# Kernel tuning notes

Measured on AMD Instinct MI355X. Metric: run time of the kernel, lower is better.

## Reference

```python
import jax, jax.numpy as jnp
import numpy as np

N = 10000        # nodes
F_IN = 128       # node features (data.num_node_features)
OUT = 16         # out_channels
H = 32           # attention heads
C1 = 4 * OUT     # hidden per-head dim (4*out_channels)
E = 80000        # directed edges
EPS = 1e-5       # BatchNorm eps
NEG = 0.2        # GATConv LeakyReLU negative_slope


def _gat(x, src, dst, W, a_s, a_d, b, n, C):
    # PyG GATConv, shared lin, concat=False (mean over heads)
    h = (x @ W).reshape(n, H, C)                    # [n,H,C]
    e_src = jnp.sum(h * a_s, -1)                    # [n,H] (alpha from x_j)
    e_dst = jnp.sum(h * a_d, -1)                    # [n,H] (alpha from x_i)
    e = jax.nn.leaky_relu(e_src[src] + e_dst[dst], NEG)     # [E',H]
    m = jax.ops.segment_max(e, dst, num_segments=n)         # segment softmax
    p = jnp.exp(e - m[dst])
    z = jax.ops.segment_sum(p, dst, num_segments=n)
    alpha = p / z[dst]
    out = jax.ops.segment_sum(alpha[:, :, None] * h[src], dst, num_segments=n)
    return out.mean(1) + b                          # mean over heads + bias


def _bn(x, g, b, m, v):  # eval-mode BatchNorm1d (running stats)
    return (x - m) * g / jnp.sqrt(v + EPS) + b


def setup_inputs():
    k = jax.random.split(jax.random.key(0), 40)
    rn = lambda i, s, sc=0.1: jax.random.normal(k[i], s, jnp.float32) * sc
    d = {"x": jax.random.normal(k[0], (N, F_IN), jnp.float32),
         "edge_index": jax.random.randint(k[1], (2, E), 0, N, jnp.int32)}
    # 4 GATConv layers
    d.update(W1=rn(2, (F_IN, H * C1)), as1=rn(3, (H, C1)), ad1=rn(4, (H, C1)), b1=rn(5, (C1,)))
    d.update(W2=rn(6, (C1, H * OUT)), as2=rn(7, (H, OUT)), ad2=rn(8, (H, OUT)), b2=rn(9, (OUT,)))
    d.update(W3=rn(10, (F_IN, H * C1)), as3=rn(11, (H, C1)), ad3=rn(12, (H, C1)), b3=rn(13, (C1,)))
    d.update(W4=rn(14, (C1, H * OUT)), as4=rn(15, (H, OUT)), ad4=rn(16, (H, OUT)), b4=rn(17, (OUT,)))
    # ResidualNetwork(1 block): 1x1 Conv1d over L=1 == matmul
    d.update(rwa=rn(18, (F_IN, OUT)), rba=rn(19, (OUT,)),
             bn1g=jnp.ones(OUT), bn1b=jnp.zeros(OUT), bn1m=rn(20, (OUT,)), bn1v=jnp.abs(rn(21, (OUT,))) + 1.0,
             rwb=rn(22, (OUT, OUT)), rbb=rn(23, (OUT,)),
             bn2g=jnp.ones(OUT), bn2b=jnp.zeros(OUT), bn2m=rn(24, (OUT,)), bn2v=jnp.abs(rn(25, (OUT,))) + 1.0,
             wsc=rn(26, (F_IN, OUT)), bsc=rn(27, (OUT,)),
             bnsg=jnp.ones(OUT), bnsb=jnp.zeros(OUT), bnsm=rn(28, (OUT,)), bnsv=jnp.abs(rn(29, (OUT,))) + 1.0,
             wfc=rn(30, (OUT, OUT)), bfc=rn(31, (OUT,)))
    return d


def reference(x, edge_index, W1, as1, ad1, b1, W2, as2, ad2, b2,
              W3, as3, ad3, b3, W4, as4, ad4, b4,
              rwa, rba, bn1g, bn1b, bn1m, bn1v, rwb, rbb, bn2g, bn2b, bn2m, bn2v,
              wsc, bsc, bnsg, bnsb, bnsm, bnsv, wfc, bfc):
    n = x.shape[0]
    loops = jnp.arange(n, dtype=edge_index.dtype)  # add_self_loops=True
    s2t_src = jnp.concatenate([edge_index[0], loops])  # flow source_to_target
    s2t_dst = jnp.concatenate([edge_index[1], loops])
    t2s_src = jnp.concatenate([edge_index[1], loops])  # flow target_to_source
    t2s_dst = jnp.concatenate([edge_index[0], loops])
    # dropout in original is unassigned (no-op); eval mode assumed
    x_s = jax.nn.elu(_gat(x, s2t_src, s2t_dst, W1, as1, ad1, b1, n, C1))
    x_in = jax.nn.elu(_gat(x_s, s2t_src, s2t_dst, W2, as2, ad2, b2, n, OUT))
    x_t = jax.nn.elu(_gat(x, t2s_src, t2s_dst, W3, as3, ad3, b3, n, C1))
    x_out = jax.nn.elu(_gat(x_t, t2s_src, t2s_dst, W4, as4, ad4, b4, n, OUT))
    # ResidualNetwork: block + identity avg-pool (L=1) + fc
    h = jax.nn.relu(_bn(x @ rwa + rba, bn1g, bn1b, bn1m, bn1v))
    h = _bn(h @ rwb + rbb, bn2g, bn2b, bn2m, bn2v)
    sc = _bn(x @ wsc + bsc, bnsg, bnsb, bnsm, bnsv)
    x_self = jax.nn.relu(h + sc) @ wfc + bfc
    return (x_in, x_out, x_self)
```

## Files before the change

### kernel.cpp

```cpp
#include <hip/hip_runtime.h>
#include <stdint.h>

__device__ __forceinline__ float bf2f(unsigned short u) {
  union { unsigned int i; float f; } v; v.i = ((unsigned int)u) << 16; return v.f;
}
__device__ __forceinline__ unsigned short f2bf(float f) {
  union { float f; unsigned int i; } v; v.f = f;
  unsigned int i = v.i;
  unsigned int r = (i + 0x7fffu + ((i >> 16) & 1u)) >> 16;
  return (unsigned short)r;
}

typedef __bf16 bf16x8 __attribute__((ext_vector_type(8)));
typedef float f32x4 __attribute__((ext_vector_type(4)));
typedef float f32x2 __attribute__((ext_vector_type(2)));
union ABfrag { int4 i4; bf16x8 v; };

#if __has_builtin(__builtin_amdgcn_cvt_pk_fp8_f32) && __has_builtin(__builtin_amdgcn_cvt_pk_f32_fp8)
#define HW_FP8 1
#else
#define HW_FP8 0
#endif

__device__ __forceinline__ unsigned char f2fp8_sw(float f) {
  union { float f; unsigned int u; } v; v.f = f;
  unsigned int s = (v.u >> 24) & 0x80;
  float a = fabsf(f);
  if (a >= 448.f) return (unsigned char)(s | 0x7E);
  v.f = a;
  int ex = (int)(v.u >> 23);
  unsigned int man = v.u & 0x7FFFFFu;
  if (ex >= 121) {
    unsigned int val = ((unsigned int)(ex - 120) << 3) | (man >> 20);
    unsigned int rem = man & 0xFFFFFu;
    if (rem > 0x80000u || (rem == 0x80000u && (val & 1))) val++;
    if (val > 0x7E) val = 0x7E;
    return (unsigned char)(s | val);
  }
  int q = (int)(a * 512.f + 0.5f);
  if (q > 8) q = 8;
  return (unsigned char)(s | (unsigned int)q);
}
__device__ __forceinline__ float fp8dec_sw(unsigned char c) {
  unsigned int e = (c >> 3) & 15u, m = c & 7u;
  float v;
  if (e) { union { unsigned int u; float f; } x; x.u = ((e + 120) << 23) | (m << 20); v = x.f; }
  else v = (float)m * 0.001953125f;
  return (c & 0x80) ? -v : v;
}
__device__ __forceinline__ unsigned int pack4_fp8(float a0, float a1, float a2, float a3) {
#if HW_FP8
  int dw = __builtin_amdgcn_cvt_pk_fp8_f32(a0, a1, 0, false);
  dw = __builtin_amdgcn_cvt_pk_fp8_f32(a2, a3, dw, true);
  return (unsigned int)dw;
#else
  return (unsigned)f2fp8_sw(a0) | ((unsigned)f2fp8_sw(a1) << 8) |
         ((unsigned)f2fp8_sw(a2) << 16) | ((unsigned)f2fp8_sw(a3) << 24);
#endif
}
__device__ __forceinline__ unsigned int bytesel4(uint4 v, int rr) {
#if __has_builtin(__builtin_amdgcn_perm)
  unsigned s = (unsigned)rr | ((unsigned)(rr + 4) << 8);
  unsigned p01 = __builtin_amdgcn_perm(v.y, v.x, s);
  unsigned p23 = __builtin_amdgcn_perm(v.w, v.z, s);
  return __builtin_amdgcn_perm(p23, p01, 0x05040100u);
#else
  int sh = rr * 8;
  return ((v.x >> sh) & 0xFFu) | (((v.y >> sh) & 0xFFu) << 8) |
         (((v.z >> sh) & 0xFFu) << 16) | (((v.w >> sh) & 0xFFu) << 24);
#endif
}
__device__ __forceinline__ void dec16p(int4 g, f32x2 o[8]) {
#if HW_FP8
  o[0] = __builtin_amdgcn_cvt_pk_f32_fp8(g.x, false);
  o[1] = __builtin_amdgcn_cvt_pk_f32_fp8(g.x, true);
  o[2] = __builtin_amdgcn_cvt_pk_f32_fp8(g.y, false);
  o[3] = __builtin_amdgcn_cvt_pk_f32_fp8(g.y, true);
  o[4] = __builtin_amdgcn_cvt_pk_f32_fp8(g.z, false);
  o[5] = __builtin_amdgcn_cvt_pk_f32_fp8(g.z, true);
  o[6] = __builtin_amdgcn_cvt_pk_f32_fp8(g.w, false);
  o[7] = __builtin_amdgcn_cvt_pk_f32_fp8(g.w, true);
#else
  unsigned int w[4] = {(unsigned)g.x, (unsigned)g.y, (unsigned)g.z, (unsigned)g.w};
#pragma unroll
  for (int d = 0; d < 4; ++d) {
    unsigned int x = w[d];
    o[d * 2 + 0] = (f32x2){fp8dec_sw((unsigned char)(x & 0xFF)),
                           fp8dec_sw((unsigned char)((x >> 8) & 0xFF))};
    o[d * 2 + 1] = (f32x2){fp8dec_sw((unsigned char)((x >> 16) & 0xFF)),
                           fp8dec_sw((unsigned char)((x >> 24) & 0xFF))};
  }
#endif
}

__device__ __forceinline__ float lrelu_clamp(float e) {
  e = (e > 0.f) ? e : 0.2f * e;
  return fminf(e, 80.f);
}

__global__ __launch_bounds__(256) void k_detect(const unsigned int* __restrict__ x, int* flag,
                                                int* __restrict__ degAB, int ndeg2) {
  if (blockIdx.x == 0) {
    __shared__ int cnt;
    if (threadIdx.x == 0) cnt = 0;
    __syncthreads();
    int c = 0;
    for (int i = threadIdx.x; i < 1024; i += 256) {
      unsigned int lo = x[i] & 0xFFFFu;
      int ex = (int)((lo >> 7) & 0xFF);
      if (ex >= 100 && ex <= 140) c++;
    }
    atomicAdd(&cnt, c);
    __syncthreads();
    if (threadIdx.x == 0) flag[0] = (cnt > 600) ? 1 : 0;
    return;
  }
  for (int idx = (blockIdx.x - 1) * 256 + threadIdx.x; idx < ndeg2; idx += 8 * 256) degAB[idx] = 0;
}

struct PrepDesc {
  const void* csrc[32]; float* cdst[32]; int cn[32];
  const void* x; float* xc; unsigned short* xp;
  const void* W1; const void* W2; const void* W3; const void* W4;
  unsigned short* P1; unsigned short* P2; unsigned short* P3; unsigned short* P4;
  int* degAB;
  const int* ei;
  const void* av[4];
  float* wa[4];
  int nxb, xtotal, ctotal, E, nn;
};
__global__ __launch_bounds__(256) void k_prep(PrepDesc d, const int* __restrict__ flag) {
  int isbf = *flag;
  int b = blockIdx.x;
  if (b < d.nxb) {
    int t8 = b * 256 + threadIdx.x;
    int i8 = t8 * 8;
    if (i8 < d.xtotal) {
      float v[8];
      if (isbf) {
        int4 raw = *(const int4*)((const unsigned short*)d.x + i8);
        const unsigned short* u = (const unsigned short*)&raw;
#pragma unroll
        for (int j = 0; j < 8; ++j) v[j] = bf2f(u[j]);
      } else {
        float4 f0 = *(const float4*)((const float*)d.x + i8);
        float4 f1 = *(const float4*)((const float*)d.x + i8 + 4);
        v[0] = f0.x; v[1] = f0.y; v[2] = f0.z; v[3] = f0.w;
        v[4] = f1.x; v[5] = f1.y; v[6] = f1.z; v[7] = f1.w;
      }
      *(float4*)(d.xc + i8)     = (float4){v[0], v[1], v[2], v[3]};
      *(float4*)(d.xc + i8 + 4) = (float4){v[4], v[5], v[6], v[7]};
      int row = i8 >> 7, c0 = i8 & 127;
      int tm = row >> 4, mr = row & 15;
      int s = c0 >> 5, quad = (c0 >> 3) & 3;
      unsigned short o[8];
#pragma unroll
      for (int j = 0; j < 8; ++j) o[j] = f2bf(v[j]);
      size_t idx = (((size_t)tm * 4 + s) * 64 + quad * 16 + mr) * 8;
      *(int4*)(d.xp + idx) = *(const int4*)o;
    }
    return;
  }
  b -= d.nxb;
  if (b < 288) {
    int u = b * 256 + threadIdx.x;
    const void* W; unsigned short* P; int K, N, lu;
    if (u < 32768)      { W = d.W1; P = d.P1; K = 128; N = 2048; lu = u; }
    else if (u < 36864) { W = d.W2; P = d.P2; K = 64;  N = 512;  lu = u - 32768; }
    else if (u < 69632) { W = d.W3; P = d.P3; K = 128; N = 2048; lu = u - 36864; }
    else                { W = d.W4; P = d.P4; K = 64;  N = 512;  lu = u - 69632; }
    int ksteps = K >> 5;
    int g = lu / (ksteps * 64);
    int rem = lu - g * (ksteps * 64);
    int s = rem >> 6, lane = rem & 63;
    int mr = lane & 15, quad = lane >> 4;
    int col = g * 16 + mr;
    int kbase = s * 32 + quad * 8;
#pragma unroll
    for (int j = 0; j < 8; ++j) {
      size_t src = (size_t)(kbase + j) * N + col;
      float v = isbf ? bf2f(((const unsigned short*)W)[src]) : ((const float*)W)[src];
      P[(size_t)lu * 8 + j] = f2bf(v);
    }
    return;
  }
  b -= 288;
  if (b < 4) {
    for (int idx = b * 256 + threadIdx.x; idx < d.ctotal; idx += 4 * 256) {
      int t = 0, off = idx;
      while (off >= d.cn[t]) { off -= d.cn[t]; ++t; }
      float v = isbf ? bf2f(((const unsigned short*)d.csrc[t])[off])
                     : ((const float*)d.csrc[t])[off];
      d.cdst[t][off] = v;
    }
    return;
  }
  b -= 4;
  {
    int degblks = (d.E + 255) >> 8;
    if (b < degblks) {
      int e = b * 256 + threadIdx.x;
      if (e < d.E) {
        atomicAdd(&d.degAB[d.ei[d.E + e]], 1);
        atomicAdd(&d.degAB[d.nn + d.ei[e]], 1);
      }
      return;
    }
    b -= degblks;
  }
  {
    int m = b >> 4, kb = b & 15;
    const void* W = (m < 2) ? d.W1 : d.W3;
    const void* A = d.av[m];
    float* out = d.wa[m];
    int k = kb * 8 + (threadIdx.x >> 5);
    int h = threadIdx.x & 31;
    size_t wbase = (size_t)k * 2048 + h * 64;
    size_t abase = (size_t)h * 64;
    float acc = 0.f;
    if (isbf) {
      const unsigned short* Wb = (const unsigned short*)W;
      const unsigned short* Ab = (const unsigned short*)A;
#pragma unroll
      for (int v8 = 0; v8 < 8; ++v8) {
        int4 wv = *(const int4*)(Wb + wbase + v8 * 8);
        int4 av = *(const int4*)(Ab + abase + v8 * 8);
        const unsigned short* wu = (const unsigned short*)&wv;
        const unsigned short* au = (const unsigned short*)&av;
#pragma unroll
        for (int j = 0; j < 8; ++j) acc += bf2f(wu[j]) * bf2f(au[j]);
      }
    } else {
      const float* Wf = (const float*)W;
      const float* Af = (const float*)A;
#pragma unroll
      for (int v4 = 0; v4 < 16; ++v4) {
        float4 wv = *(const float4*)(Wf + wbase + v4 * 4);
        float4 av = *(const float4*)(Af + abase + v4 * 4);
        acc += wv.x * av.x + wv.y * av.y + wv.z * av.z + wv.w * av.w;
      }
    }
    out[k * 32 + h] = acc;
  }
}

__global__ __launch_bounds__(1024) void k_exscan2(const int* __restrict__ degA, const int* __restrict__ degB,
                                                  int* __restrict__ rowA, int* __restrict__ rowB,
                                                  int* __restrict__ colA, int* __restrict__ colB,
                                                  int* __restrict__ curA, int* __restrict__ curB, int n) {
  const int* deg = (blockIdx.x == 0) ? degA : degB;
  int* row = (blockIdx.x == 0) ? rowA : rowB;
  int* colx = (blockIdx.x == 0) ? colA : colB;
  int* curx = (blockIdx.x == 0) ? curA : curB;
  __shared__ int wsum[16], wbase[16];
  __shared__ int carry;
  if (threadIdx.x == 0) carry = 0;
  __syncthreads();
  int lane = threadIdx.x & 63, w = threadIdx.x >> 6;
  int chunks = (n + 1023) >> 10;
  for (int ch = 0; ch < chunks; ++ch) {
    int i = (ch << 10) + threadIdx.x;
    int v = (i < n) ? deg[i] : 0;
    int sc = v;
#pragma unroll
    for (int o = 1; o < 64; o <<= 1) { int t = __shfl_up(sc, o); if (lane >= o) sc += t; }
    if (lane == 63) wsum[w] = sc;
    __syncthreads();
    if (threadIdx.x < 16) {
      int v2 = wsum[threadIdx.x], s2 = v2;
#pragma unroll
      for (int o = 1; o < 16; o <<= 1) { int t = __shfl_up(s2, o); if (lane >= o) s2 += t; }
      wbase[threadIdx.x] = s2 - v2;
      if (threadIdx.x == 15) wsum[15] = s2;
    }
    __syncthreads();
    if (i < n) {
      int rv = carry + wbase[w] + (sc - v) + i;
      row[i] = rv;
      colx[rv] = i;
      curx[i] = rv + 1;
    }
    __syncthreads();
    if (threadIdx.x == 0) carry += wsum[15];
    __syncthreads();
  }
  if (threadIdx.x == 0) row[n] = carry + n;
}

struct AuxDesc {
  int resblks, E;
  const int* ei; int* colA; int* colB; int* curA; int* curB;
  const float* xc;
  const float* rp[20];
  const float* wa[4];
  float* es1; float* ed1; float* es3; float* ed3;
  void* outbase; size_t eoff; int n;
  const int* flag;
};
__global__ __launch_bounds__(256) void k_aux(AuxDesc d) {
  __shared__ struct { float xs[16][128]; float ha[16][16]; float tt[16][16]; } sm;
  int b = blockIdx.x;
  if (b < d.resblks) {
    int nodebase = b * 16;
    for (int t = threadIdx.x; t < 16 * 128; t += 256)
      sm.xs[t >> 7][t & 127] = d.xc[(size_t)(nodebase + (t >> 7)) * 128 + (t & 127)];
    __syncthreads();
    int ni = threadIdx.x >> 4, c = threadIdx.x & 15;
    {
      const float* w0 = d.wa[0]; const float* w1 = d.wa[1];
      const float* w2 = d.wa[2]; const float* w3 = d.wa[3];
      float a0 = 0.f, a1 = 0.f, a2 = 0.f, a3 = 0.f, a4 = 0.f, a5 = 0.f, a6 = 0.f, a7 = 0.f;
#pragma unroll 4
      for (int k = 0; k < 128; ++k) {
        float xv = sm.xs[ni][k];
        int o = k * 32 + c;
        a0 += xv * w0[o]; a1 += xv * w0[o + 16];
        a2 += xv * w1[o]; a3 += xv * w1[o + 16];
        a4 += xv * w2[o]; a5 += xv * w2[o + 16];
        a6 += xv * w3[o]; a7 += xv * w3[o + 16];
      }
      int row = nodebase + ni;
      d.es1[row * 32 + c] = a0; d.es1[row * 32 + c + 16] = a1;
      d.ed1[row * 32 + c] = a2; d.ed1[row * 32 + c + 16] = a3;
      d.es3[row * 32 + c] = a4; d.es3[row * 32 + c + 16] = a5;
      d.ed3[row * 32 + c] = a6; d.ed3[row * 32 + c + 16] = a7;
    }
    const float* rwa = d.rp[0]; const float* rba = d.rp[1];
    const float* bn1g = d.rp[2]; const float* bn1b = d.rp[3];
    const float* bn1m = d.rp[4]; const float* bn1v = d.rp[5];
    const float* rwb = d.rp[6]; const float* rbb = d.rp[7];
    const float* bn2g = d.rp[8]; const float* bn2b = d.rp[9];
    const float* bn2m = d.rp[10]; const float* bn2v = d.rp[11];
    const float* wsc = d.rp[12]; const float* bsc = d.rp[13];
    const float* bnsg = d.rp[14]; const float* bnsb = d.rp[15];
    const float* bnsm = d.rp[16]; const float* bnsv = d.rp[17];
    const float* wfc = d.rp[18]; const float* bfc = d.rp[19];
    float ya = 0.f, ysc = 0.f;
#pragma unroll 8
    for (int k = 0; k < 128; ++k) {
      float xv = sm.xs[ni][k];
      ya  += xv * rwa[k * 16 + c];
      ysc += xv * wsc[k * 16 + c];
    }
    ya += rba[c]; ysc += bsc[c];
    float s1 = bn1g[c] * rsqrtf(bn1v[c] + 1e-5f);
    ya = (ya - bn1m[c]) * s1 + bn1b[c];
    ya = fmaxf(ya, 0.f);
    float ss = bnsg[c] * rsqrtf(bnsv[c] + 1e-5f);
    ysc = (ysc - bnsm[c]) * ss + bnsb[c];
    sm.ha[ni][c] = ya;
    __syncthreads();
    float h2 = rbb[c];
#pragma unroll
    for (int k = 0; k < 16; ++k) h2 += sm.ha[ni][k] * rwb[k * 16 + c];
    float s2 = bn2g[c] * rsqrtf(bn2v[c] + 1e-5f);
    h2 = (h2 - bn2m[c]) * s2 + bn2b[c];
    sm.tt[ni][c] = fmaxf(h2 + ysc, 0.f);
    __syncthreads();
    float o = bfc[c];
#pragma unroll
    for (int k = 0; k < 16; ++k) o += sm.tt[ni][k] * wfc[k * 16 + c];
    size_t oo = d.eoff + (size_t)(nodebase + ni) * 16 + c;
    if (*d.flag) ((unsigned short*)d.outbase)[oo] = f2bf(o);
    else         ((float*)d.outbase)[oo] = o;
    return;
  }
  b -= d.resblks;
  {
    int e = b * 256 + threadIdx.x;
    if (e < d.E) {
      int s = d.ei[e], dd = d.ei[d.E + e];
      d.colA[atomicAdd(&d.curA[dd], 1)] = s;
      d.colB[atomicAdd(&d.curB[s], 1)] = dd;
    }
  }
}

#define TILE_DW 288
template<int CH, int KSTEPS>
__device__ __forceinline__ void mm_es64_body(int rg, int cg, int MT,
    const unsigned short* __restrict__ Ap, const unsigned short* __restrict__ Bp,
    unsigned char* __restrict__ C, const float* __restrict__ a_s, const float* __restrict__ a_d,
    float* __restrict__ es, float* __restrict__ ed, int N, unsigned int* tile) {
  const int TI = KSTEPS * 64;
  int vt = MT - rg * 4; if (vt > 4) vt = 4;
  int wid = threadIdx.x >> 6;
  int tn = cg * 4 + wid;
  int lane = threadIdx.x & 63;
  int mr = lane & 15, quad = lane >> 4;
  const int4* ap = (const int4*)(Ap + (size_t)rg * 4 * TI * 8) + lane;
  const unsigned short* bp = Bp + ((size_t)tn * 4 * KSTEPS) * 512 + lane * 8;
  unsigned int* twave = tile + wid * TILE_DW;
  f32x4 acc[4][4];
#pragma unroll
  for (int rt = 0; rt < 4; ++rt)
#pragma unroll
    for (int nt = 0; nt < 4; ++nt) acc[rt][nt] = (f32x4){0.f, 0.f, 0.f, 0.f};
#pragma unroll
  for (int s = 0; s < KSTEPS; ++s) {
    ABfrag bfr[4];
#pragma unroll
    for (int nt = 0; nt < 4; ++nt) bfr[nt].i4 = *(const int4*)(bp + (size_t)(nt * KSTEPS + s) * 512);
    ABfrag afr[4];
#pragma unroll
    for (int rt = 0; rt < 4; ++rt) {
      int rti = (rt < vt) ? rt : 0;
      afr[rt].i4 = ap[rti * TI + s * 64];
    }
#pragma unroll
    for (int nt = 0; nt < 4; ++nt)
#pragma unroll
      for (int rt = 0; rt < 4; ++rt)
        acc[rt][nt] = __builtin_amdgcn_mfma_f32_16x16x32_bf16(afr[rt].v, bfr[nt].v, acc[rt][nt], 0, 0, 0);
  }
  int r16 = lane >> 2, seg = lane & 3;
  int qr = r16 >> 2, rr = r16 & 3;
#pragma unroll
  for (int rt = 0; rt < 4; ++rt) {
    if (rt < vt) {
      int tm = rg * 4 + rt;
#pragma unroll
      for (int nt = 0; nt < 4; ++nt) {
        unsigned int dwv = pack4_fp8(acc[rt][nt][0], acc[rt][nt][1], acc[rt][nt][2], acc[rt][nt][3]);
        twave[quad * 72 + nt * 16 + mr] = dwv;
      }
      unsigned int out[4];
#pragma unroll
      for (int w = 0; w < 4; ++w) {
        uint4 v = *(const uint4*)&twave[qr * 72 + seg * 16 + 4 * w];
        out[w] = bytesel4(v, rr);
      }
      *(int4*)(C + (size_t)(tm * 16 + r16) * N + tn * 64 + seg * 16) = *(const int4*)out;
    }
  }
  if (CH == 16) {
    float ws[4], wd[4];
#pragma unroll
    for (int nt = 0; nt < 4; ++nt) {
      ws[nt] = a_s[(tn * 4 + nt) * 16 + mr];
      wd[nt] = a_d[(tn * 4 + nt) * 16 + mr];
    }
#pragma unroll
    for (int rt = 0; rt < 4; ++rt) {
      if (rt < vt) {
        int tm = rg * 4 + rt;
        float pes[4][4], ped[4][4];
#pragma unroll
        for (int nt = 0; nt < 4; ++nt)
#pragma unroll
          for (int r = 0; r < 4; ++r) { pes[nt][r] = acc[rt][nt][r] * ws[nt]; ped[nt][r] = acc[rt][nt][r] * wd[nt]; }
#pragma unroll
        for (int m = 1; m < 16; m <<= 1)
#pragma unroll
          for (int nt = 0; nt < 4; ++nt)
#pragma unroll
            for (int r = 0; r < 4; ++r) {
              pes[nt][r] += __shfl_xor(pes[nt][r], m);
              ped[nt][r] += __shfl_xor(ped[nt][r], m);
            }
        if (mr == 0) {
#pragma unroll
          for (int nt = 0; nt < 4; ++nt)
#pragma unroll
            for (int r = 0; r < 4; ++r) {
              int row = tm * 16 + quad * 4 + r;
              es[row * 32 + tn * 4 + nt] = pes[nt][r];
              ed[row * 32 + tn * 4 + nt] = ped[nt][r];
            }
        }
      }
    }
  }
}

struct MMDesc {
  const unsigned short* Ap;
  const unsigned short* B1; const unsigned short* B3;
  unsigned char* C1; unsigned char* C3;
  int mmblks, mt;
};
__global__ __launch_bounds__(256) void k_mm13(MMDesc d) {
  __shared__ unsigned int tile[4 * TILE_DW];
  int b = blockIdx.x;
  if (b < d.mmblks) {
    mm_es64_body<64,4>(b >> 3, b & 7, d.mt, d.Ap, d.B1, d.C1, nullptr, nullptr, nullptr, nullptr, 2048, tile);
    return;
  }
  b -= d.mmblks;
  mm_es64_body<64,4>(b >> 3, b & 7, d.mt, d.Ap, d.B3, d.C3, nullptr, nullptr, nullptr, nullptr, 2048, tile);
}

__global__ __launch_bounds__(256) void k_g64(const unsigned char* __restrict__ h1,
                                             const unsigned char* __restrict__ h3,
                                             const float* __restrict__ es1, const float* __restrict__ ed1,
                                             const float* __restrict__ es3, const float* __restrict__ ed3,
                                             const int* __restrict__ rowA, const int* __restrict__ colA,
                                             const int* __restrict__ rowB, const int* __restrict__ colB,
                                             const float* __restrict__ b1, const float* __restrict__ b3,
                                             unsigned short* __restrict__ xsp, unsigned short* __restrict__ xtp,
                                             int n, int gb) {
  int b = blockIdx.x;
  const unsigned char* h; const float *es, *ed, *bias; const int *rowp, *col; unsigned short* outp;
  if (b < gb) { h = h1; es = es1; ed = ed1; rowp = rowA; col = colA; bias = b1; outp = xsp; }
  else { b -= gb; h = h3; es = es3; ed = ed3; rowp = rowB; col = colB; bias = b3; outp = xtp; }
  int wid = threadIdx.x >> 6, lane = threadIdx.x & 63;
  int i = b * 4 + wid;
  if (i >= n) return;
  int hd0 = lane >> 2, hd1 = 16 + hd0;
  float e0 = ed[i * 32 + hd0];
  float e1 = ed[i * 32 + hd1];
  int beg = rowp[i], end = rowp[i + 1];
  int deg = end - beg;
  int colv = (lane < deg) ? col[beg + lane] : 0;
  f32x2 acc0[8], acc1[8];
#pragma unroll
  for (int k = 0; k < 8; ++k) { acc0[k] = (f32x2){0.f, 0.f}; acc1[k] = (f32x2){0.f, 0.f}; }
  float Z0 = 0.f, Z1 = 0.f;
  int s0 = __shfl(colv, 0);
  const int4* hp0 = (const int4*)(h + (size_t)s0 * 2048);
  int4 ng0 = hp0[lane];
  int4 ng1 = hp0[64 + lane];
  float na = es[s0 * 32 + hd0];
  float nb = es[s0 * 32 + hd1];
  for (int j = 0; j < deg; ++j) {
    int4 g0 = ng0, g1 = ng1;
    float ea = na, eb = nb;
    int jn = j + 1;
    if (jn < deg) {
      int sn = (jn < 64) ? __shfl(colv, jn) : col[beg + jn];
      const int4* hq = (const int4*)(h + (size_t)sn * 2048);
      ng0 = hq[lane];
      ng1 = hq[64 + lane];
      na = es[sn * 32 + hd0];
      nb = es[sn * 32 + hd1];
    }
    float q0 = __expf(lrelu_clamp(ea + e0));
    float q1 = __expf(lrelu_clamp(eb + e1));
    Z0 += q0; Z1 += q1;
    f32x2 d0[8], d1[8];
    dec16p(g0, d0); dec16p(g1, d1);
    f32x2 q0v = (f32x2){q0, q0}, q1v = (f32x2){q1, q1};
#pragma unroll
    for (int k = 0; k < 8; ++k) {
      acc0[k] = __builtin_elementwise_fma(q0v, d0[k], acc0[k]);
      acc1[k] = __builtin_elementwise_fma(q1v, d1[k], acc1[k]);
    }
  }
  float zi0 = 1.0f / Z0, zi1 = 1.0f / Z1;
  f32x2 zi0v = (f32x2){zi0, zi0}, zi1v = (f32x2){zi1, zi1};
  f32x2 v2[8];
#pragma unroll
  for (int k = 0; k < 8; ++k)
    v2[k] = __builtin_elementwise_fma(acc1[k], zi1v, acc0[k] * zi0v);
#pragma unroll
  for (int m = 4; m < 64; m <<= 1)
#pragma unroll
    for (int k = 0; k < 8; ++k) {
      v2[k].x += __shfl_xor(v2[k].x, m);
      v2[k].y += __shfl_xor(v2[k].y, m);
    }
  if (lane < 4) {
    float v[16];
#pragma unroll
    for (int k = 0; k < 8; ++k) { v[2 * k] = v2[k].x; v[2 * k + 1] = v2[k].y; }
    int tm = i >> 4, mr = i & 15;
    unsigned short ob[16];
#pragma unroll
    for (int k = 0; k < 16; ++k) {
      float t = v[k] * (1.f / 32.f) + bias[lane * 16 + k];
      t = (t > 0.f) ? t : (__expf(t) - 1.f);
      ob[k] = f2bf(t);
    }
    int s0w = lane >> 1;
#pragma unroll
    for (int g2 = 0; g2 < 2; ++g2) {
      size_t idx = (((size_t)tm * 2 + s0w) * 64 + ((lane & 1) * 2 + g2) * 16 + mr) * 8;
      *(int4*)(outp + idx) = *(const int4*)(ob + g2 * 8);
    }
  }
}

__global__ __launch_bounds__(256) void k_mm24(const unsigned short* __restrict__ xsp,
                                              const unsigned short* __restrict__ xtp,
                                              const unsigned short* __restrict__ W2p,
                                              const unsigned short* __restrict__ W4p,
                                              unsigned char* __restrict__ h2, unsigned char* __restrict__ h4,
                                              const float* __restrict__ as2, const float* __restrict__ ad2,
                                              const float* __restrict__ as4, const float* __restrict__ ad4,
                                              float* __restrict__ es2, float* __restrict__ ed2,
                                              float* __restrict__ es4, float* __restrict__ ed4,
                                              int mmblks, int mt) {
  __shared__ unsigned int tile[4 * TILE_DW];
  int b = blockIdx.x;
  if (b < mmblks)
    mm_es64_body<16,2>(b >> 1, b & 1, mt, xsp, W2p, h2, as2, ad2, es2, ed2, 512, tile);
  else {
    b -= mmblks;
    mm_es64_body<16,2>(b >> 1, b & 1, mt, xtp, W4p, h4, as4, ad4, es4, ed4, 512, tile);
  }
}

__global__ __launch_bounds__(256) void k_g16(const unsigned char* __restrict__ h2,
                                             const unsigned char* __restrict__ h4,
                                             const float* __restrict__ es2, const float* __restrict__ ed2,
                                             const float* __restrict__ es4, const float* __restrict__ ed4,
                                             const int* __restrict__ rowA, const int* __restrict__ colA,
                                             const int* __restrict__ rowB, const int* __restrict__ colB,
                                             const float* __restrict__ b2, const float* __restrict__ b4,
                                             void* __restrict__ outbase, int n, int gb,
                                             const int* __restrict__ flag) {
  int b = blockIdx.x;
  const unsigned char* h; const float *es, *ed, *bias; const int *rowp, *col; size_t eoff;
  if (b < gb) { h = h2; es = es2; ed = ed2; rowp = rowA; col = colA; bias = b2; eoff = 0; }
  else { b -= gb; h = h4; es = es4; ed = ed4; rowp = rowB; col = colB; bias = b4; eoff = (size_t)n * 16; }
  int wid = threadIdx.x >> 6, lane = threadIdx.x & 63;
  int i = b * 4 + wid;
  if (i >= n) return;
  int hh = lane & 31, j2 = lane >> 5;
  float ev = ed[i * 32 + hh];
  int beg = rowp[i], end = rowp[i + 1];
  int deg = end - beg;
  int colv = (lane < deg) ? col[beg + lane] : 0;
  f32x2 acc[8];
#pragma unroll
  for (int k = 0; k < 8; ++k) acc[k] = (f32x2){0.f, 0.f};
  float Z = 0.f;
  int j = j2;
  int4 ng = (int4){0, 0, 0, 0};
  float ne = 0.f;
  if (j < deg) {
    int s = __shfl(colv, j);
    ng = ((const int4*)(h + (size_t)s * 512))[hh];
    ne = es[s * 32 + hh];
  }
  for (; j < deg; j += 2) {
    int4 g = ng; float ee = ne;
    int jn = j + 2;
    if (jn < deg) {
      int sn = (jn < 64) ? __shfl(colv, jn) : col[beg + jn];
      ng = ((const int4*)(h + (size_t)sn * 512))[hh];
      ne = es[sn * 32 + hh];
    }
    float q = __expf(lrelu_clamp(ee + ev));
    Z += q;
    f32x2 d[8];
    dec16p(g, d);
    f32x2 qv = (f32x2){q, q};
#pragma unroll
    for (int k = 0; k < 8; ++k) acc[k] = __builtin_elementwise_fma(qv, d[k], acc[k]);
  }
  Z += __shfl_xor(Z, 32);
  float zi = 1.0f / Z;
  f32x2 ziv = (f32x2){zi, zi};
  f32x2 v2[8];
#pragma unroll
  for (int k = 0; k < 8; ++k) v2[k] = acc[k] * ziv;
#pragma unroll
  for (int m = 1; m < 64; m <<= 1)
#pragma unroll
    for (int k = 0; k < 8; ++k) {
      v2[k].x += __shfl_xor(v2[k].x, m);
      v2[k].y += __shfl_xor(v2[k].y, m);
    }
  if (lane == 0) {
    float v[16];
#pragma unroll
    for (int k = 0; k < 8; ++k) { v[2 * k] = v2[k].x; v[2 * k + 1] = v2[k].y; }
    int isbf = *flag;
    if (isbf) {
      unsigned short ob[16];
#pragma unroll
      for (int k = 0; k < 16; ++k) {
        float t = v[k] * (1.f / 32.f) + bias[k];
        t = (t > 0.f) ? t : (__expf(t) - 1.f);
        ob[k] = f2bf(t);
      }
      unsigned short* o = (unsigned short*)outbase + eoff + (size_t)i * 16;
      *(int4*)o = *(const int4*)ob;
      *(int4*)(o + 8) = *(const int4*)(ob + 8);
    } else {
      float* o = (float*)outbase + eoff + (size_t)i * 16;
#pragma unroll
      for (int k = 0; k < 16; ++k) {
        float t = v[k] * (1.f / 32.f) + bias[k];
        t = (t > 0.f) ? t : (__expf(t) - 1.f);
        o[k] = t;
      }
    }
  }
}

extern "C" void kernel_launch(void* const* d_in, const int* in_sizes, int n_in,
                              void* d_out, int out_size, void* d_ws, size_t ws_size,
                              hipStream_t stream) {
  const int n = in_sizes[0] / 128;
  const int E = in_sizes[1] / 2;
  const int* ei = (const int*)d_in[1];

  char* wsp = (char*)d_ws; size_t off = 0;
  auto alloc = [&](size_t bytes) -> void* {
    void* p = wsp + off; off = (off + bytes + 255) & ~(size_t)255; return p;
  };
  int* flag = (int*)alloc(4);
  float* xc = (float*)alloc((size_t)n * 128 * 4);
  unsigned short* xp = (unsigned short*)alloc((size_t)n * 128 * 2);
  unsigned short* W1p = (unsigned short*)alloc((size_t)2048 * 128 * 2);
  unsigned short* W2p = (unsigned short*)alloc((size_t)512 * 64 * 2);
  unsigned short* W3p = (unsigned short*)alloc((size_t)2048 * 128 * 2);
  unsigned short* W4p = (unsigned short*)alloc((size_t)512 * 64 * 2);
  unsigned char* h1 = (unsigned char*)alloc((size_t)n * 2048);
  unsigned char* h3 = (unsigned char*)alloc((size_t)n * 2048);
  unsigned char* h2 = (unsigned char*)alloc((size_t)n * 512);
  unsigned char* h4 = (unsigned char*)alloc((size_t)n * 512);
  float* es1 = (float*)alloc((size_t)n * 32 * 4);
  float* ed1 = (float*)alloc((size_t)n * 32 * 4);
  float* es3 = (float*)alloc((size_t)n * 32 * 4);
  float* ed3 = (float*)alloc((size_t)n * 32 * 4);
  float* es2 = (float*)alloc((size_t)n * 32 * 4);
  float* ed2 = (float*)alloc((size_t)n * 32 * 4);
  float* es4 = (float*)alloc((size_t)n * 32 * 4);
  float* ed4 = (float*)alloc((size_t)n * 32 * 4);
  unsigned short* xsp = (unsigned short*)alloc((size_t)n * 64 * 2);
  unsigned short* xtp = (unsigned short*)alloc((size_t)n * 64 * 2);
  int* rowA = (int*)alloc((size_t)(n + 1) * 4);
  int* rowB = (int*)alloc((size_t)(n + 1) * 4);
  int* colA = (int*)alloc((size_t)(E + n) * 4);
  int* colB = (int*)alloc((size_t)(E + n) * 4);
  int* degAB = (int*)alloc((size_t)2 * n * 4);
  int* degA = degAB, * degB = degAB + n;
  int* curA = (int*)alloc((size_t)n * 4);
  int* curB = (int*)alloc((size_t)n * 4);
  float* was1 = (float*)alloc((size_t)128 * 32 * 4);
  float* wad1 = (float*)alloc((size_t)128 * 32 * 4);
  float* was3 = (float*)alloc((size_t)128 * 32 * 4);
  float* wad3 = (float*)alloc((size_t)128 * 32 * 4);

  static const int cidx[32] = {3,4,5, 7,8,9, 11,12,13, 15,16,17,
                               18,19,20,21,22,23,24,25,26,27,28,29,
                               30,31,32,33,34,35,36,37};
  PrepDesc pd;
  float* canon[38] = {nullptr};
  pd.ctotal = 0;
  for (int t = 0; t < 32; ++t) {
    int ii = cidx[t];
    canon[ii] = (float*)alloc((size_t)in_sizes[ii] * 4);
    pd.csrc[t] = d_in[ii];
    pd.cdst[t] = canon[ii];
    pd.cn[t] = in_sizes[ii];
    pd.ctotal += in_sizes[ii];
  }
  pd.x = d_in[0]; pd.xc = xc; pd.xp = xp;
  pd.W1 = d_in[2]; pd.W2 = d_in[6]; pd.W3 = d_in[10]; pd.W4 = d_in[14];
  pd.P1 = W1p; pd.P2 = W2p; pd.P3 = W3p; pd.P4 = W4p;
  pd.degAB = degAB;
  pd.ei = ei;
  pd.av[0] = d_in[3]; pd.av[1] = d_in[4]; pd.av[2] = d_in[11]; pd.av[3] = d_in[12];
  pd.wa[0] = was1; pd.wa[1] = wad1; pd.wa[2] = was3; pd.wa[3] = wad3;
  pd.nxb = (n * 128 / 8 + 255) / 256;
  pd.xtotal = n * 128;
  pd.E = E;
  pd.nn = n;
  (void)ws_size; (void)n_in; (void)out_size;

  const int degblks = (E + 255) / 256;

  k_detect<<<9, 256, 0, stream>>>((const unsigned int*)d_in[0], flag, degAB, 2 * n);
  k_prep<<<pd.nxb + 288 + 4 + degblks + 64, 256, 0, stream>>>(pd, flag);
  k_exscan2<<<2, 1024, 0, stream>>>(degA, degB, rowA, rowB, colA, colB, curA, curB, n);

  const int mt = n / 16;
  const int nrg = (mt + 3) / 4;
  const int mmblks64 = nrg * 8;
  const int mmblks16 = nrg * 2;
  const int gb = (n + 3) / 4;

  AuxDesc ad;
  ad.resblks = mt; ad.E = E;
  ad.ei = ei; ad.colA = colA; ad.colB = colB; ad.curA = curA; ad.curB = curB;
  ad.xc = xc;
  for (int t = 0; t < 20; ++t) ad.rp[t] = canon[18 + t];
  ad.wa[0] = was1; ad.wa[1] = wad1; ad.wa[2] = was3; ad.wa[3] = wad3;
  ad.es1 = es1; ad.ed1 = ed1; ad.es3 = es3; ad.ed3 = ed3;
  ad.outbase = d_out; ad.eoff = (size_t)2 * n * 16; ad.n = n; ad.flag = flag;
  k_aux<<<mt + degblks, 256, 0, stream>>>(ad);

  MMDesc md;
  md.Ap = xp; md.B1 = W1p; md.B3 = W3p; md.C1 = h1; md.C3 = h3;
  md.mmblks = mmblks64; md.mt = mt;
  k_mm13<<<2 * mmblks64, 256, 0, stream>>>(md);

  k_g64<<<2 * gb, 256, 0, stream>>>(h1, h3, es1, ed1, es3, ed3,
                                    rowA, colA, rowB, colB,
                                    canon[5], canon[13], xsp, xtp, n, gb);
  k_mm24<<<2 * mmblks16, 256, 0, stream>>>(xsp, xtp, W2p, W4p, h2, h4,
                                           canon[7], canon[8], canon[15], canon[16],
                                           es2, ed2, es4, ed4, mmblks16, mt);
  k_g16<<<2 * gb, 256, 0, stream>>>(h2, h4, es2, ed2, es4, ed4,
                                    rowA, colA, rowB, colB,
                                    canon[9], canon[17], d_out, n, gb, flag);
}
```

Baseline: 324.8 us.

## Merge aux work into mm13 launch, split g64 heads across two waves

Folds the residual-network, attention-logit and CSR-scatter work from k_aux into the k_mm13 launch as extra block ranges sharing a union of shared memory, which removes one kernel launch and lets that work overlap with the matmul blocks. The k_g64 gather now assigns two waves per node, each handling 16 heads, and combines the two halves through shared memory. This halves per-wave register and accumulator pressure and raises parallelism, at the cost of a __syncthreads and an extra LDS reduction. The parameter-copy phase in k_prep also now uses one block per tensor instead of a strided loop with a tensor-index search.

```diff
diff --git a/kernel.cpp b/kernel.cpp
--- a/kernel.cpp
+++ b/kernel.cpp
@@ -185,17 +185,19 @@
     return;
   }
   b -= 288;
-  if (b < 4) {
-    for (int idx = b * 256 + threadIdx.x; idx < d.ctotal; idx += 4 * 256) {
-      int t = 0, off = idx;
-      while (off >= d.cn[t]) { off -= d.cn[t]; ++t; }
-      float v = isbf ? bf2f(((const unsigned short*)d.csrc[t])[off])
-                     : ((const float*)d.csrc[t])[off];
-      d.cdst[t][off] = v;
+  if (b < 32) {
+    int t = b;
+    int nels = d.cn[t];
+    const void* src = d.csrc[t];
+    float* dst = d.cdst[t];
+    for (int idx = threadIdx.x; idx < nels; idx += 256) {
+      float v = isbf ? bf2f(((const unsigned short*)src)[idx])
+                     : ((const float*)src)[idx];
+      dst[idx] = v;
     }
     return;
   }
-  b -= 4;
+  b -= 32;
   {
     int degblks = (d.E + 255) >> 8;
     if (b < degblks) {
@@ -287,95 +289,6 @@
   if (threadIdx.x == 0) row[n] = carry + n;
 }
 
-struct AuxDesc {
-  int resblks, E;
-  const int* ei; int* colA; int* colB; int* curA; int* curB;
-  const float* xc;
-  const float* rp[20];
-  const float* wa[4];
-  float* es1; float* ed1; float* es3; float* ed3;
-  void* outbase; size_t eoff; int n;
-  const int* flag;
-};
-__global__ __launch_bounds__(256) void k_aux(AuxDesc d) {
-  __shared__ struct { float xs[16][128]; float ha[16][16]; float tt[16][16]; } sm;
-  int b = blockIdx.x;
-  if (b < d.resblks) {
-    int nodebase = b * 16;
-    for (int t = threadIdx.x; t < 16 * 128; t += 256)
-      sm.xs[t >> 7][t & 127] = d.xc[(size_t)(nodebase + (t >> 7)) * 128 + (t & 127)];
-    __syncthreads();
-    int ni = threadIdx.x >> 4, c = threadIdx.x & 15;
-    {
-      const float* w0 = d.wa[0]; const float* w1 = d.wa[1];
-      const float* w2 = d.wa[2]; const float* w3 = d.wa[3];
-      float a0 = 0.f, a1 = 0.f, a2 = 0.f, a3 = 0.f, a4 = 0.f, a5 = 0.f, a6 = 0.f, a7 = 0.f;
-#pragma unroll 4
-      for (int k = 0; k < 128; ++k) {
-        float xv = sm.xs[ni][k];
-        int o = k * 32 + c;
-        a0 += xv * w0[o]; a1 += xv * w0[o + 16];
-        a2 += xv * w1[o]; a3 += xv * w1[o + 16];
-        a4 += xv * w2[o]; a5 += xv * w2[o + 16];
-        a6 += xv * w3[o]; a7 += xv * w3[o + 16];
-      }
-      int row = nodebase + ni;
-      d.es1[row * 32 + c] = a0; d.es1[row * 32 + c + 16] = a1;
-      d.ed1[row * 32 + c] = a2; d.ed1[row * 32 + c + 16] = a3;
-      d.es3[row * 32 + c] = a4; d.es3[row * 32 + c + 16] = a5;
-      d.ed3[row * 32 + c] = a6; d.ed3[row * 32 + c + 16] = a7;
-    }
-    const float* rwa = d.rp[0]; const float* rba = d.rp[1];
-    const float* bn1g = d.rp[2]; const float* bn1b = d.rp[3];
-    const float* bn1m = d.rp[4]; const float* bn1v = d.rp[5];
-    const float* rwb = d.rp[6]; const float* rbb = d.rp[7];
-    const float* bn2g = d.rp[8]; const float* bn2b = d.rp[9];
-    const float* bn2m = d.rp[10]; const float* bn2v = d.rp[11];
-    const float* wsc = d.rp[12]; const float* bsc = d.rp[13];
-    const float* bnsg = d.rp[14]; const float* bnsb = d.rp[15];
-    const float* bnsm = d.rp[16]; const float* bnsv = d.rp[17];
-    const float* wfc = d.rp[18]; const float* bfc = d.rp[19];
-    float ya = 0.f, ysc = 0.f;
-#pragma unroll 8
-    for (int k = 0; k < 128; ++k) {
-      float xv = sm.xs[ni][k];
-      ya  += xv * rwa[k * 16 + c];
-      ysc += xv * wsc[k * 16 + c];
-    }
-    ya += rba[c]; ysc += bsc[c];
-    float s1 = bn1g[c] * rsqrtf(bn1v[c] + 1e-5f);
-    ya = (ya - bn1m[c]) * s1 + bn1b[c];
-    ya = fmaxf(ya, 0.f);
-    float ss = bnsg[c] * rsqrtf(bnsv[c] + 1e-5f);
-    ysc = (ysc - bnsm[c]) * ss + bnsb[c];
-    sm.ha[ni][c] = ya;
-    __syncthreads();
-    float h2 = rbb[c];
-#pragma unroll
-    for (int k = 0; k < 16; ++k) h2 += sm.ha[ni][k] * rwb[k * 16 + c];
-    float s2 = bn2g[c] * rsqrtf(bn2v[c] + 1e-5f);
-    h2 = (h2 - bn2m[c]) * s2 + bn2b[c];
-    sm.tt[ni][c] = fmaxf(h2 + ysc, 0.f);
-    __syncthreads();
-    float o = bfc[c];
-#pragma unroll
-    for (int k = 0; k < 16; ++k) o += sm.tt[ni][k] * wfc[k * 16 + c];
-    size_t oo = d.eoff + (size_t)(nodebase + ni) * 16 + c;
-    if (*d.flag) ((unsigned short*)d.outbase)[oo] = f2bf(o);
-    else         ((float*)d.outbase)[oo] = o;
-    return;
-  }
-  b -= d.resblks;
-  {
-    int e = b * 256 + threadIdx.x;
-    if (e < d.E) {
-      int s = d.ei[e], dd = d.ei[d.E + e];
-      d.colA[atomicAdd(&d.curA[dd], 1)] = s;
-      d.colB[atomicAdd(&d.curB[s], 1)] = dd;
-    }
-  }
-}
-
 #define TILE_DW 288
 template<int CH, int KSTEPS>
 __device__ __forceinline__ void mm_es64_body(int rg, int cg, int MT,
@@ -473,21 +386,108 @@
   }
 }
 
-struct MMDesc {
+union SM13 {
+  struct { float xs[16][128]; float ha[16][16]; float tt[16][16]; } res;
+  unsigned int tile[4 * TILE_DW];
+};
+struct MM13XDesc {
+  int resblks, sblks, mmblks, mt, E;
+  const int* ei; int* colA; int* colB; int* curA; int* curB;
+  const float* xc;
+  const float* rp[20];
+  const float* wa[4];
+  float* es1; float* ed1; float* es3; float* ed3;
+  void* outbase; size_t eoff; int n;
+  const int* flag;
   const unsigned short* Ap;
   const unsigned short* B1; const unsigned short* B3;
   unsigned char* C1; unsigned char* C3;
-  int mmblks, mt;
 };
-__global__ __launch_bounds__(256) void k_mm13(MMDesc d) {
-  __shared__ unsigned int tile[4 * TILE_DW];
+__global__ __launch_bounds__(256) void k_mm13x(MM13XDesc d) {
+  __shared__ SM13 sm;
   int b = blockIdx.x;
+  if (b < d.resblks) {
+    int nodebase = b * 16;
+    for (int t = threadIdx.x; t < 16 * 128; t += 256)
+      sm.res.xs[t >> 7][t & 127] = d.xc[(size_t)(nodebase + (t >> 7)) * 128 + (t & 127)];
+    __syncthreads();
+    int ni = threadIdx.x >> 4, c = threadIdx.x & 15;
+    {
+      const float* w0 = d.wa[0]; const float* w1 = d.wa[1];
+      const float* w2 = d.wa[2]; const float* w3 = d.wa[3];
+      float a0 = 0.f, a1 = 0.f, a2 = 0.f, a3 = 0.f, a4 = 0.f, a5 = 0.f, a6 = 0.f, a7 = 0.f;
+#pragma unroll 4
+      for (int k = 0; k < 128; ++k) {
+        float xv = sm.res.xs[ni][k];
+        int o = k * 32 + c;
+        a0 += xv * w0[o]; a1 += xv * w0[o + 16];
+        a2 += xv * w1[o]; a3 += xv * w1[o + 16];
+        a4 += xv * w2[o]; a5 += xv * w2[o + 16];
+        a6 += xv * w3[o]; a7 += xv * w3[o + 16];
+      }
+      int row = nodebase + ni;
+      d.es1[row * 32 + c] = a0; d.es1[row * 32 + c + 16] = a1;
+      d.ed1[row * 32 + c] = a2; d.ed1[row * 32 + c + 16] = a3;
+      d.es3[row * 32 + c] = a4; d.es3[row * 32 + c + 16] = a5;
+      d.ed3[row * 32 + c] = a6; d.ed3[row * 32 + c + 16] = a7;
+    }
+    const float* rwa = d.rp[0]; const float* rba = d.rp[1];
+    const float* bn1g = d.rp[2]; const float* bn1b = d.rp[3];
+    const float* bn1m = d.rp[4]; const float* bn1v = d.rp[5];
+    const float* rwb = d.rp[6]; const float* rbb = d.rp[7];
+    const float* bn2g = d.rp[8]; const float* bn2b = d.rp[9];
+    const float* bn2m = d.rp[10]; const float* bn2v = d.rp[11];
+    const float* wsc = d.rp[12]; const float* bsc = d.rp[13];
+    const float* bnsg = d.rp[14]; const float* bnsb = d.rp[15];
+    const float* bnsm = d.rp[16]; const float* bnsv = d.rp[17];
+    const float* wfc = d.rp[18]; const float* bfc = d.rp[19];
+    float ya = 0.f, ysc = 0.f;
+#pragma unroll 8
+    for (int k = 0; k < 128; ++k) {
+      float xv = sm.res.xs[ni][k];
+      ya  += xv * rwa[k * 16 + c];
+      ysc += xv * wsc[k * 16 + c];
+    }
+    ya += rba[c]; ysc += bsc[c];
+    float s1 = bn1g[c] * rsqrtf(bn1v[c] + 1e-5f);
+    ya = (ya - bn1m[c]) * s1 + bn1b[c];
+    ya = fmaxf(ya, 0.f);
+    float ss = bnsg[c] * rsqrtf(bnsv[c] + 1e-5f);
+    ysc = (ysc - bnsm[c]) * ss + bnsb[c];
+    sm.res.ha[ni][c] = ya;
+    __syncthreads();
+    float h2 = rbb[c];
+#pragma unroll
+    for (int k = 0; k < 16; ++k) h2 += sm.res.ha[ni][k] * rwb[k * 16 + c];
+    float s2 = bn2g[c] * rsqrtf(bn2v[c] + 1e-5f);
+    h2 = (h2 - bn2m[c]) * s2 + bn2b[c];
+    sm.res.tt[ni][c] = fmaxf(h2 + ysc, 0.f);
+    __syncthreads();
+    float o = bfc[c];
+#pragma unroll
+    for (int k = 0; k < 16; ++k) o += sm.res.tt[ni][k] * wfc[k * 16 + c];
+    size_t oo = d.eoff + (size_t)(nodebase + ni) * 16 + c;
+    if (*d.flag) ((unsigned short*)d.outbase)[oo] = f2bf(o);
+    else         ((float*)d.outbase)[oo] = o;
+    return;
+  }
+  b -= d.resblks;
+  if (b < d.sblks) {
+    int e = b * 256 + threadIdx.x;
+    if (e < d.E) {
+      int s = d.ei[e], dd = d.ei[d.E + e];
+      d.colA[atomicAdd(&d.curA[dd], 1)] = s;
+      d.colB[atomicAdd(&d.curB[s], 1)] = dd;
+    }
+    return;
+  }
+  b -= d.sblks;
   if (b < d.mmblks) {
-    mm_es64_body<64,4>(b >> 3, b & 7, d.mt, d.Ap, d.B1, d.C1, nullptr, nullptr, nullptr, nullptr, 2048, tile);
+    mm_es64_body<64,4>(b >> 3, b & 7, d.mt, d.Ap, d.B1, d.C1, nullptr, nullptr, nullptr, nullptr, 2048, sm.tile);
     return;
   }
   b -= d.mmblks;
-  mm_es64_body<64,4>(b >> 3, b & 7, d.mt, d.Ap, d.B3, d.C3, nullptr, nullptr, nullptr, nullptr, 2048, tile);
+  mm_es64_body<64,4>(b >> 3, b & 7, d.mt, d.Ap, d.B3, d.C3, nullptr, nullptr, nullptr, nullptr, 2048, sm.tile);
 }
 
 __global__ __launch_bounds__(256) void k_g64(const unsigned char* __restrict__ h1,
@@ -499,59 +499,56 @@
                                              const float* __restrict__ b1, const float* __restrict__ b3,
                                              unsigned short* __restrict__ xsp, unsigned short* __restrict__ xtp,
                                              int n, int gb) {
+  __shared__ float part[2][2][64];
   int b = blockIdx.x;
   const unsigned char* h; const float *es, *ed, *bias; const int *rowp, *col; unsigned short* outp;
   if (b < gb) { h = h1; es = es1; ed = ed1; rowp = rowA; col = colA; bias = b1; outp = xsp; }
   else { b -= gb; h = h3; es = es3; ed = ed3; rowp = rowB; col = colB; bias = b3; outp = xtp; }
   int wid = threadIdx.x >> 6, lane = threadIdx.x & 63;
-  int i = b * 4 + wid;
-  if (i >= n) return;
-  int hd0 = lane >> 2, hd1 = 16 + hd0;
-  float e0 = ed[i * 32 + hd0];
-  float e1 = ed[i * 32 + hd1];
-  int beg = rowp[i], end = rowp[i + 1];
-  int deg = end - beg;
+  int nb = wid >> 1, half = wid & 1;
+  int i = b * 2 + nb;
+  bool active = (i < n);
+  int hd = half * 16 + (lane >> 2);
+  float e0 = 0.f;
+  int beg = 0, deg = 0;
+  if (active) {
+    e0 = ed[i * 32 + hd];
+    beg = rowp[i];
+    deg = rowp[i + 1] - beg;
+  }
   int colv = (lane < deg) ? col[beg + lane] : 0;
-  f32x2 acc0[8], acc1[8];
-#pragma unroll
-  for (int k = 0; k < 8; ++k) { acc0[k] = (f32x2){0.f, 0.f}; acc1[k] = (f32x2){0.f, 0.f}; }
-  float Z0 = 0.f, Z1 = 0.f;
-  int s0 = __shfl(colv, 0);
-  const int4* hp0 = (const int4*)(h + (size_t)s0 * 2048);
-  int4 ng0 = hp0[lane];
-  int4 ng1 = hp0[64 + lane];
-  float na = es[s0 * 32 + hd0];
-  float nb = es[s0 * 32 + hd1];
-  for (int j = 0; j < deg; ++j) {
-    int4 g0 = ng0, g1 = ng1;
-    float ea = na, eb = nb;
-    int jn = j + 1;
-    if (jn < deg) {
-      int sn = (jn < 64) ? __shfl(colv, jn) : col[beg + jn];
-      const int4* hq = (const int4*)(h + (size_t)sn * 2048);
-      ng0 = hq[lane];
-      ng1 = hq[64 + lane];
-      na = es[sn * 32 + hd0];
-      nb = es[sn * 32 + hd1];
-    }
-    float q0 = __expf(lrelu_clamp(ea + e0));
-    float q1 = __expf(lrelu_clamp(eb + e1));
-    Z0 += q0; Z1 += q1;
-    f32x2 d0[8], d1[8];
-    dec16p(g0, d0); dec16p(g1, d1);
-    f32x2 q0v = (f32x2){q0, q0}, q1v = (f32x2){q1, q1};
-#pragma unroll
-    for (int k = 0; k < 8; ++k) {
-      acc0[k] = __builtin_elementwise_fma(q0v, d0[k], acc0[k]);
-      acc1[k] = __builtin_elementwise_fma(q1v, d1[k], acc1[k]);
-    }
-  }
-  float zi0 = 1.0f / Z0, zi1 = 1.0f / Z1;
-  f32x2 zi0v = (f32x2){zi0, zi0}, zi1v = (f32x2){zi1, zi1};
+  f32x2 acc[8];
+#pragma unroll
+  for (int k = 0; k < 8; ++k) acc[k] = (f32x2){0.f, 0.f};
+  float Z = 0.f;
+  if (active) {
+    int s0 = __shfl(colv, 0);
+    const int4* hp = (const int4*)(h + (size_t)s0 * 2048 + (size_t)half * 1024);
+    int4 ng = hp[lane];
+    float ne = es[s0 * 32 + hd];
+    for (int j = 0; j < deg; ++j) {
+      int4 g = ng; float ee = ne;
+      int jn = j + 1;
+      if (jn < deg) {
+        int sn = (jn < 64) ? __shfl(colv, jn) : col[beg + jn];
+        const int4* hq = (const int4*)(h + (size_t)sn * 2048 + (size_t)half * 1024);
+        ng = hq[lane];
+        ne = es[sn * 32 + hd];
+      }
+      float q = __expf(lrelu_clamp(ee + e0));
+      Z += q;
+      f32x2 d[8];
+      dec16p(g, d);
+      f32x2 qv = (f32x2){q, q};
+#pragma unroll
+      for (int k = 0; k < 8; ++k) acc[k] = __builtin_elementwise_fma(qv, d[k], acc[k]);
+    }
+  }
+  float zi = active ? (1.0f / Z) : 0.f;
+  f32x2 ziv = (f32x2){zi, zi};
   f32x2 v2[8];
 #pragma unroll
-  for (int k = 0; k < 8; ++k)
-    v2[k] = __builtin_elementwise_fma(acc1[k], zi1v, acc0[k] * zi0v);
+  for (int k = 0; k < 8; ++k) v2[k] = acc[k] * ziv;
 #pragma unroll
   for (int m = 4; m < 64; m <<= 1)
 #pragma unroll
@@ -560,9 +557,16 @@
       v2[k].y += __shfl_xor(v2[k].y, m);
     }
   if (lane < 4) {
+#pragma unroll
+    for (int k = 0; k < 8; ++k)
+      *(float2*)&part[nb][half][lane * 16 + 2 * k] = (float2){v2[k].x, v2[k].y};
+  }
+  __syncthreads();
+  if (half == 0 && lane < 4 && active) {
     float v[16];
 #pragma unroll
-    for (int k = 0; k < 8; ++k) { v[2 * k] = v2[k].x; v[2 * k + 1] = v2[k].y; }
+    for (int k = 0; k < 16; ++k)
+      v[k] = part[nb][0][lane * 16 + k] + part[nb][1][lane * 16 + k];
     int tm = i >> 4, mr = i & 15;
     unsigned short ob[16];
 #pragma unroll
@@ -765,33 +769,30 @@
   const int degblks = (E + 255) / 256;
 
   k_detect<<<9, 256, 0, stream>>>((const unsigned int*)d_in[0], flag, degAB, 2 * n);
-  k_prep<<<pd.nxb + 288 + 4 + degblks + 64, 256, 0, stream>>>(pd, flag);
+  k_prep<<<pd.nxb + 288 + 32 + degblks + 64, 256, 0, stream>>>(pd, flag);
   k_exscan2<<<2, 1024, 0, stream>>>(degA, degB, rowA, rowB, colA, colB, curA, curB, n);
 
   const int mt = n / 16;
   const int nrg = (mt + 3) / 4;
   const int mmblks64 = nrg * 8;
   const int mmblks16 = nrg * 2;
+  const int gb2 = (n + 1) / 2;
   const int gb = (n + 3) / 4;
 
-  AuxDesc ad;
-  ad.resblks = mt; ad.E = E;
-  ad.ei = ei; ad.colA = colA; ad.colB = colB; ad.curA = curA; ad.curB = curB;
-  ad.xc = xc;
-  for (int t = 0; t < 20; ++t) ad.rp[t] = canon[18 + t];
-  ad.wa[0] = was1; ad.wa[1] = wad1; ad.wa[2] = was3; ad.wa[3] = wad3;
-  ad.es1 = es1; ad.ed1 = ed1; ad.es3 = es3; ad.ed3 = ed3;
-  ad.outbase = d_out; ad.eoff = (size_t)2 * n * 16; ad.n = n; ad.flag = flag;
-  k_aux<<<mt + degblks, 256, 0, stream>>>(ad);
-
-  MMDesc md;
+  MM13XDesc md;
+  md.resblks = mt; md.sblks = degblks; md.mmblks = mmblks64; md.mt = mt; md.E = E;
+  md.ei = ei; md.colA = colA; md.colB = colB; md.curA = curA; md.curB = curB;
+  md.xc = xc;
+  for (int t = 0; t < 20; ++t) md.rp[t] = canon[18 + t];
+  md.wa[0] = was1; md.wa[1] = wad1; md.wa[2] = was3; md.wa[3] = wad3;
+  md.es1 = es1; md.ed1 = ed1; md.es3 = es3; md.ed3 = ed3;
+  md.outbase = d_out; md.eoff = (size_t)2 * n * 16; md.n = n; md.flag = flag;
   md.Ap = xp; md.B1 = W1p; md.B3 = W3p; md.C1 = h1; md.C3 = h3;
-  md.mmblks = mmblks64; md.mt = mt;
-  k_mm13<<<2 * mmblks64, 256, 0, stream>>>(md);
-
-  k_g64<<<2 * gb, 256, 0, stream>>>(h1, h3, es1, ed1, es3, ed3,
-                                    rowA, colA, rowB, colB,
-                                    canon[5], canon[13], xsp, xtp, n, gb);
+  k_mm13x<<<mt + degblks + 2 * mmblks64, 256, 0, stream>>>(md);
+
+  k_g64<<<2 * gb2, 256, 0, stream>>>(h1, h3, es1, ed1, es3, ed3,
+                                     rowA, colA, rowB, colB,
+                                     canon[5], canon[13], xsp, xtp, n, gb2);
   k_mm24<<<2 * mmblks16, 256, 0, stream>>>(xsp, xtp, W2p, W4p, h2, h4,
                                            canon[7], canon[8], canon[15], canon[16],
                                            es2, ed2, es4, ed4, mmblks16, mt);
```

After: 314.2 us. 1.03x faster.
